# Kernel tuning notes

Hardware: AMD Instinct MI355X
Metric: run time of the kernel (lower is better)

Reference implementation:

```python
import jax, jax.numpy as jnp
import numpy as np

D = 1024      # model_dim
H = 2048      # expert hidden_dim
E = 8         # num routed experts
TOP_K = 2
N_SHARED = 1
B, S = 2, 1024


def setup_inputs() -> dict:
    key = jax.random.key(0)
    ks = jax.random.split(key, 12)
    sc = 0.02
    return {
        "hidden": jax.random.normal(ks[0], (B, S, D), jnp.float32),
        # router Linear(D -> E); stored as [in, out]
        "router_w": jax.random.normal(ks[1], (D, E), jnp.float32) * sc,
        "router_b": jnp.zeros((E,), jnp.float32),
        # shared expert (1): Linear(D->H), Linear(H->D)
        "sw1": jax.random.normal(ks[2], (D, H), jnp.float32) * sc,
        "sb1": jnp.zeros((H,), jnp.float32),
        "sw2": jax.random.normal(ks[3], (H, D), jnp.float32) * sc,
        "sb2": jnp.zeros((D,), jnp.float32),
        # routed experts, stacked over E
        "rw1": jax.random.normal(ks[4], (E, D, H), jnp.float32) * sc,
        "rb1": jnp.zeros((E, H), jnp.float32),
        "rw2": jax.random.normal(ks[5], (E, H, D), jnp.float32) * sc,
        "rb2": jnp.zeros((E, D), jnp.float32),
    }


def reference(hidden, router_w, router_b, sw1, sb1, sw2, sb2, rw1, rb1, rw2, rb2):
    b, s, d = hidden.shape
    T = b * s
    flat = hidden.reshape(T, d)                              # [T, D]

    # --- router ---
    router_logits = flat @ router_w + router_b               # [T, E]
    router_probs = jax.nn.softmax(router_logits, axis=-1)
    topk_probs, topk_idx = jax.lax.top_k(router_probs, TOP_K)  # [T, K]

    # per-(token, expert) mixing weight: sum of top-k probs that hit expert e
    weights = jnp.zeros_like(router_probs).at[
        jnp.arange(T)[:, None], topk_idx
    ].add(topk_probs)                                        # [T, E]

    # --- shared expert(s) (1 expert -> mean == itself) ---
    sh = jax.nn.gelu(flat @ sw1 + sb1, approximate=False)    # [T, H]
    shared_out = (sh @ sw2 + sb2) / N_SHARED                 # [T, D]

    # --- routed experts: dense all-expert eval weighted by routing weights ---
    # (identical math to the gather/FFN/index_add loop: weight is 0 for
    #  tokens not routed to expert e)
    h1 = jax.nn.gelu(jnp.einsum('td,edh->teh', flat, rw1) + rb1[None],
                     approximate=False)                      # [T, E, H]
    expert_out = jnp.einsum('teh,ehd->ted', h1, rw2) + rb2[None]  # [T, E, D]
    mixed = jnp.einsum('ted,te->td', expert_out, weights)    # [T, D]

    return (shared_out + mixed).reshape(b, s, d)
```

## Files before the change

### kernel.cpp

```cpp
#include <hip/hip_runtime.h>
#include <hip/hip_bf16.h>

#define T_TOK 2048
#define DDIM  1024
#define HDIM  2048
#define NEXP  8
#define NSEG  9

typedef unsigned short u16;
typedef __attribute__((ext_vector_type(4))) float f32x4;
typedef __attribute__((ext_vector_type(8))) short bf16x8;
typedef __attribute__((ext_vector_type(4))) unsigned short u16x4;

__device__ __forceinline__ u16 f2bf(float x) {
  union { float f; unsigned int u; } v; v.f = x;
  unsigned int r = v.u + 0x7fffu + ((v.u >> 16) & 1u);
  return (u16)(r >> 16);
}
__device__ __forceinline__ float gelu_exact(float x) {
  return 0.5f * x * (1.0f + erff(x * 0.70710678118654752f));
}
__device__ __forceinline__ int swz4(int row) {
  return (row & 3) ^ ((row >> 2) & 3);
}

__device__ __forceinline__ void gload16(const void* g, void* l) {
  __builtin_amdgcn_global_load_lds(
      (const __attribute__((address_space(1))) unsigned int*)g,
      (__attribute__((address_space(3))) unsigned int*)l, 16, 0, 0);
}

__global__ __launch_bounds__(256) void router_kernel(
    const float* __restrict__ x, const float* __restrict__ rw,
    const float* __restrict__ rb, u16* __restrict__ xb,
    float* __restrict__ weights, int* __restrict__ counts,
    int* __restrict__ lists)
{
  int wv = threadIdx.x >> 6, lane = threadIdx.x & 63;
  int t = blockIdx.x * 4 + wv;
  const float* xrow = x + (size_t)t * DDIM;
  float acc[NEXP];
#pragma unroll
  for (int e = 0; e < NEXP; e++) acc[e] = 0.f;
#pragma unroll
  for (int i = 0; i < 4; i++) {
    int d0 = i * 256 + lane * 4;
    f32x4 xv = *(const f32x4*)(xrow + d0);
    u16x4 pk;
#pragma unroll
    for (int j = 0; j < 4; j++) {
      float xs = xv[j];
      pk[j] = f2bf(xs);
      const float* wr = rw + (size_t)(d0 + j) * NEXP;
#pragma unroll
      for (int e = 0; e < NEXP; e++) acc[e] = fmaf(xs, wr[e], acc[e]);
    }
    *(u16x4*)(xb + (size_t)t * DDIM + d0) = pk;
  }
#pragma unroll
  for (int off = 32; off >= 1; off >>= 1)
#pragma unroll
    for (int e = 0; e < NEXP; e++) acc[e] += __shfl_xor(acc[e], off);

  if (lane == 0) {
    float lg[NEXP], mx = -1e30f;
#pragma unroll
    for (int e = 0; e < NEXP; e++) { lg[e] = acc[e] + rb[e]; mx = fmaxf(mx, lg[e]); }
    float p[NEXP], s = 0.f;
#pragma unroll
    for (int e = 0; e < NEXP; e++) { p[e] = expf(lg[e] - mx); s += p[e]; }
    float inv = 1.0f / s;
#pragma unroll
    for (int e = 0; e < NEXP; e++) p[e] *= inv;
    int i1 = 0;
#pragma unroll
    for (int e = 1; e < NEXP; e++) if (p[e] > p[i1]) i1 = e;
    int i2 = (i1 == 0) ? 1 : 0;
#pragma unroll
    for (int e = 0; e < NEXP; e++) if (e != i1 && p[e] > p[i2]) i2 = e;
#pragma unroll
    for (int e = 0; e < NEXP; e++)
      weights[(size_t)t * NEXP + e] = (e == i1) ? p[i1] : (e == i2) ? p[i2] : 0.f;
    int p1 = atomicAdd(counts + i1, 1); lists[i1 * T_TOK + p1] = t;
    int p2 = atomicAdd(counts + i2, 1); lists[i2 * T_TOK + p2] = t;
    lists[NEXP * T_TOK + t] = t;
  }
}

__global__ void seg_kernel(int* counts, int* segoff, int* ytab, int* nyt) {
  counts[NEXP] = T_TOK;
  int off = 0, n = 0;
  for (int e = 0; e < NSEG; e++) {
    segoff[e] = off;
    int c = counts[e];
    for (int my = 0; my * 256 < c; my++) ytab[n++] = e * 256 + my;
    off += c;
  }
  *nyt = n;
}

__global__ __launch_bounds__(256) void transpose_bf16_kernel(
    const float* __restrict__ rin, const float* __restrict__ sin_,
    u16* __restrict__ rout, u16* __restrict__ sout, int R, int C)
{
  __shared__ float tile[32][33];
  int b = blockIdx.z;
  const float* inb = (b < NEXP) ? rin + (size_t)b * R * C : sin_;
  u16* outb = (b < NEXP) ? rout + (size_t)b * R * C : sout;
  int r0 = blockIdx.y * 32, c0 = blockIdx.x * 32;
  int tx = threadIdx.x & 31, ty = threadIdx.x >> 5;
#pragma unroll
  for (int j = 0; j < 4; j++) {
    int r = ty + j * 8;
    tile[r][tx] = inb[(size_t)(r0 + r) * C + c0 + tx];
  }
  __syncthreads();
#pragma unroll
  for (int j = 0; j < 4; j++) {
    int rr = ty + j * 8;
    outb[(size_t)(c0 + rr) * R + r0 + tx] = f2bf(tile[tx][rr]);
  }
}


__global__ __launch_bounds__(512) void gemm1_kernel(
    const u16* __restrict__ Xb, const u16* __restrict__ rw1t,
    const u16* __restrict__ sw1t, const float* __restrict__ rb1,
    const float* __restrict__ sb1, const int* __restrict__ counts,
    const int* __restrict__ segoff, const int* __restrict__ lists,
    const int* __restrict__ ytab, const int* __restrict__ nyt,
    u16* __restrict__ H1)
{
  __shared__ u16 Alds[4][256 * 32];
  __shared__ u16 Blds[4][256 * 32];

  int tid = threadIdx.x, lane = tid & 63;
  int wv = tid >> 6, wm = wv >> 2, wn = wv & 3;
  int kc = lane >> 4, lr = lane & 15;

  int srow[2], soff[2];
#pragma unroll
  for (int j = 0; j < 2; j++) {
    int i = j * 512 + tid;
    srow[j] = i >> 2;
    soff[j] = (((i & 3) ^ swz4(i >> 2)) * 8);
  }
  int aoff[8], boff[4];
#pragma unroll
  for (int f = 0; f < 8; f++) {
    int ra = wm * 128 + f * 16 + lr;
    aoff[f] = ra * 32 + ((kc ^ swz4(ra)) * 8);
  }
#pragma unroll
  for (int f = 0; f < 4; f++) {
    int rb_ = wn * 64 + f * 16 + lr;
    boff[f] = rb_ * 32 + ((kc ^ swz4(rb_)) * 8);
  }

  int ntile = nyt[0] * (HDIM / 256);
  for (int t = blockIdx.x; t < ntile; t += gridDim.x) {
    int yt = t >> 3, nx = t & 7;
    int em = ytab[yt];
    int e = em >> 8, m0 = (em & 255) * 256, n0 = nx * 256;
    int cnt = counts[e];
    const u16* Bt = (e < NEXP) ? (rw1t + (size_t)e * HDIM * DDIM) : sw1t;
    const float* bias = (e < NEXP) ? (rb1 + (size_t)e * HDIM) : sb1;
    const int* list = lists + e * T_TOK;
    int seg = segoff[e];

    size_t abase[2], bbase[2];
#pragma unroll
    for (int j = 0; j < 2; j++) {
      int tok = list[min(m0 + srow[j], cnt - 1)];
      abase[j] = (size_t)tok * DDIM + soff[j];
      bbase[j] = (size_t)(n0 + srow[j]) * DDIM + soff[j];
    }

    f32x4 acc[8][4];
#pragma unroll
    for (int i = 0; i < 8; i++)
#pragma unroll
      for (int j = 0; j < 4; j++) acc[i][j] = (f32x4){0.f, 0.f, 0.f, 0.f};

    const int NS = DDIM / 32;
#pragma unroll
    for (int s = 0; s < 2; s++)
#pragma unroll
      for (int j = 0; j < 2; j++) {
        int i = j * 512 + tid;
        gload16(Xb + abase[j] + s * 32, &Alds[s][i * 8]);
        gload16(Bt + bbase[j] + s * 32, &Blds[s][i * 8]);
      }

    for (int s = 0; s < NS; s++) {
      if (s + 2 < NS) {
        int kk = (s + 2) * 32;
        int nb = (s + 2) & 3;
#pragma unroll
        for (int j = 0; j < 2; j++) {
          int i = j * 512 + tid;
          gload16(Xb + abase[j] + kk, &Alds[nb][i * 8]);
          gload16(Bt + bbase[j] + kk, &Blds[nb][i * 8]);
        }
        asm volatile("s_waitcnt vmcnt(8)" ::: "memory");
      } else if (s + 1 < NS) {
        asm volatile("s_waitcnt vmcnt(4)" ::: "memory");
      } else {
        asm volatile("s_waitcnt vmcnt(0)" ::: "memory");
      }
      __builtin_amdgcn_s_barrier();
      __builtin_amdgcn_sched_barrier(0);

      const u16* Ac = &Alds[s & 3][0];
      const u16* Bc = &Blds[s & 3][0];
      bf16x8 af[8], bfr[4];
#pragma unroll
      for (int f = 0; f < 8; f++) af[f] = *(const bf16x8*)(Ac + aoff[f]);
#pragma unroll
      for (int f = 0; f < 4; f++) bfr[f] = *(const bf16x8*)(Bc + boff[f]);
      __builtin_amdgcn_s_setprio(1);
#pragma unroll
      for (int mf = 0; mf < 8; mf++)
#pragma unroll
        for (int nf = 0; nf < 4; nf++)
          acc[mf][nf] = __builtin_amdgcn_mfma_f32_16x16x32_bf16(af[mf], bfr[nf], acc[mf][nf], 0, 0, 0);
      __builtin_amdgcn_s_setprio(0);
    }

#pragma unroll
    for (int nf = 0; nf < 4; nf++) {
      int col = n0 + wn * 64 + nf * 16 + lr;
      float b = bias[col];
#pragma unroll
      for (int mf = 0; mf < 8; mf++) {
#pragma unroll
        for (int rg = 0; rg < 4; rg++) {
          int mt = wm * 128 + mf * 16 + kc * 4 + rg;
          if (m0 + mt < cnt) {
            float v = acc[mf][nf][rg] + b;
            H1[(size_t)(seg + m0 + mt) * HDIM + col] = f2bf(gelu_exact(v));
          }
        }
      }
    }
    __builtin_amdgcn_s_barrier();
    __builtin_amdgcn_sched_barrier(0);
  }
}

__global__ __launch_bounds__(512) void gemm2_kernel(
    const u16* __restrict__ H1, const u16* __restrict__ rw2t,
    const u16* __restrict__ sw2t, const float* __restrict__ rb2,
    const float* __restrict__ sb2, const float* __restrict__ weights,
    const int* __restrict__ counts, const int* __restrict__ segoff,
    const int* __restrict__ lists, const int* __restrict__ ytab,
    const int* __restrict__ nyt, float* __restrict__ out)
{
  __shared__ u16 Alds[4][256 * 32];
  __shared__ u16 Blds[4][256 * 32];

  int tid = threadIdx.x, lane = tid & 63;
  int wv = tid >> 6, wm = wv >> 2, wn = wv & 3;
  int kc = lane >> 4, lr = lane & 15;

  int srow[2], soff[2];
#pragma unroll
  for (int j = 0; j < 2; j++) {
    int i = j * 512 + tid;
    srow[j] = i >> 2;
    soff[j] = (((i & 3) ^ swz4(i >> 2)) * 8);
  }
  int aoff[8], boff[4];
#pragma unroll
  for (int f = 0; f < 8; f++) {
    int ra = wm * 128 + f * 16 + lr;
    aoff[f] = ra * 32 + ((kc ^ swz4(ra)) * 8);
  }
#pragma unroll
  for (int f = 0; f < 4; f++) {
    int rb_ = wn * 64 + f * 16 + lr;
    boff[f] = rb_ * 32 + ((kc ^ swz4(rb_)) * 8);
  }

  int ntile = nyt[0] * (DDIM / 256) * 2;
  for (int t = blockIdx.x; t < ntile; t += gridDim.x) {
    int kh = t & 1, nx = (t >> 1) & 3, yt = t >> 3;
    int em = ytab[yt];
    int e = em >> 8, m0 = (em & 255) * 256, n0 = nx * 256;
    int cnt = counts[e];
    const u16* Bt = (e < NEXP) ? (rw2t + (size_t)e * DDIM * HDIM) : sw2t;
    const float* bias = (e < NEXP) ? (rb2 + (size_t)e * DDIM) : sb2;
    const int* list = lists + e * T_TOK;
    int seg = segoff[e];
    int k0 = kh * 1024;

    size_t abase[2], bbase[2];
#pragma unroll
    for (int j = 0; j < 2; j++) {
      abase[j] = (size_t)(seg + min(m0 + srow[j], cnt - 1)) * HDIM + k0 + soff[j];
      bbase[j] = (size_t)(n0 + srow[j]) * HDIM + k0 + soff[j];
    }

    f32x4 acc[8][4];
#pragma unroll
    for (int i = 0; i < 8; i++)
#pragma unroll
      for (int j = 0; j < 4; j++) acc[i][j] = (f32x4){0.f, 0.f, 0.f, 0.f};

    const int NS = 1024 / 32;
#pragma unroll
    for (int s = 0; s < 2; s++)
#pragma unroll
      for (int j = 0; j < 2; j++) {
        int i = j * 512 + tid;
        gload16(H1 + abase[j] + s * 32, &Alds[s][i * 8]);
        gload16(Bt + bbase[j] + s * 32, &Blds[s][i * 8]);
      }

    for (int s = 0; s < NS; s++) {
      if (s + 2 < NS) {
        int kk = (s + 2) * 32;
        int nb = (s + 2) & 3;
#pragma unroll
        for (int j = 0; j < 2; j++) {
          int i = j * 512 + tid;
          gload16(H1 + abase[j] + kk, &Alds[nb][i * 8]);
          gload16(Bt + bbase[j] + kk, &Blds[nb][i * 8]);
        }
        asm volatile("s_waitcnt vmcnt(8)" ::: "memory");
      } else if (s + 1 < NS) {
        asm volatile("s_waitcnt vmcnt(4)" ::: "memory");
      } else {
        asm volatile("s_waitcnt vmcnt(0)" ::: "memory");
      }
      __builtin_amdgcn_s_barrier();
      __builtin_amdgcn_sched_barrier(0);

      const u16* Ac = &Alds[s & 3][0];
      const u16* Bc = &Blds[s & 3][0];
      bf16x8 af[8], bfr[4];
#pragma unroll
      for (int f = 0; f < 8; f++) af[f] = *(const bf16x8*)(Ac + aoff[f]);
#pragma unroll
      for (int f = 0; f < 4; f++) bfr[f] = *(const bf16x8*)(Bc + boff[f]);
      __builtin_amdgcn_s_setprio(1);
#pragma unroll
      for (int mf = 0; mf < 8; mf++)
#pragma unroll
        for (int nf = 0; nf < 4; nf++)
          acc[mf][nf] = __builtin_amdgcn_mfma_f32_16x16x32_bf16(af[mf], bfr[nf], acc[mf][nf], 0, 0, 0);
      __builtin_amdgcn_s_setprio(0);
    }

    float biasv[4];
#pragma unroll
    for (int nf = 0; nf < 4; nf++)
      biasv[nf] = (kh == 0) ? bias[n0 + wn * 64 + nf * 16 + lr] : 0.f;

#pragma unroll
    for (int mf = 0; mf < 8; mf++) {
#pragma unroll
      for (int rg = 0; rg < 4; rg++) {
        int mt = wm * 128 + mf * 16 + kc * 4 + rg;
        int mrow = m0 + mt;
        if (mrow < cnt) {
          int tok = list[mrow];
          float w = (e < NEXP) ? weights[(size_t)tok * NEXP + e] : 1.0f;
          float* orow = out + (size_t)tok * DDIM + n0 + wn * 64 + lr;
#pragma unroll
          for (int nf = 0; nf < 4; nf++)
            atomicAdd(orow + nf * 16, w * (acc[mf][nf][rg] + biasv[nf]));
        }
      }
    }
    __builtin_amdgcn_s_barrier();
    __builtin_amdgcn_sched_barrier(0);
  }
}

extern "C" void kernel_launch(void* const* d_in, const int* in_sizes, int n_in,
                              void* d_out, int out_size, void* d_ws, size_t ws_size,
                              hipStream_t stream) {
  (void)in_sizes; (void)n_in; (void)out_size; (void)ws_size;
  const float* hidden   = (const float*)d_in[0];
  const float* router_w = (const float*)d_in[1];
  const float* router_b = (const float*)d_in[2];
  const float* sw1 = (const float*)d_in[3];
  const float* sb1 = (const float*)d_in[4];
  const float* sw2 = (const float*)d_in[5];
  const float* sb2 = (const float*)d_in[6];
  const float* rw1 = (const float*)d_in[7];
  const float* rb1 = (const float*)d_in[8];
  const float* rw2 = (const float*)d_in[9];
  const float* rb2 = (const float*)d_in[10];
  float* out = (float*)d_out;

  char* ws = (char*)d_ws;
  u16* Xb      = (u16*)(ws + 0);
  u16* rw1t    = (u16*)(ws + 4194304);
  u16* rw2t    = (u16*)(ws + 37748736);
  u16* sw1t    = (u16*)(ws + 71303168);
  u16* sw2t    = (u16*)(ws + 75497472);
  u16* H1      = (u16*)(ws + 79691776);
  float* weights = (float*)(ws + 104857600);
  int* counts  = (int*)(ws + 104923136);
  int* segoff  = (int*)(ws + 104923200);
  int* lists   = (int*)(ws + 104923264);
  int* ytab    = (int*)(ws + 104996992);
  int* nyt     = (int*)(ws + 104997632);

  hipMemsetAsync(counts, 0, 64, stream);
  hipMemsetAsync(out, 0, (size_t)T_TOK * DDIM * sizeof(float), stream);

  router_kernel<<<T_TOK / 4, 256, 0, stream>>>(hidden, router_w, router_b, Xb,
                                               weights, counts, lists);
  seg_kernel<<<1, 1, 0, stream>>>(counts, segoff, ytab, nyt);

  transpose_bf16_kernel<<<dim3(HDIM / 32, DDIM / 32, NSEG), 256, 0, stream>>>(
      rw1, sw1, rw1t, sw1t, DDIM, HDIM);
  transpose_bf16_kernel<<<dim3(DDIM / 32, HDIM / 32, NSEG), 256, 0, stream>>>(
      rw2, sw2, rw2t, sw2t, HDIM, DDIM);

  gemm1_kernel<<<256, 512, 0, stream>>>(
      Xb, rw1t, sw1t, rb1, sb1, counts, segoff, lists, ytab, nyt, H1);
  gemm2_kernel<<<256, 512, 0, stream>>>(
      H1, rw2t, sw2t, rb2, sb2, weights, counts, segoff, lists, ytab, nyt, out);
}
```

Baseline: 248.9 us.

## Pre-gather routed tokens contiguously and assign GEMM tiles per XCD

```diff
diff --git a/kernel.cpp b/kernel.cpp
--- a/kernel.cpp
+++ b/kernel.cpp
@@ -99,6 +99,22 @@
   *nyt = n;
 }
 
+__global__ __launch_bounds__(256) void gather_kernel(
+    const u16* __restrict__ xb, const int* __restrict__ lists,
+    const int* __restrict__ counts, const int* __restrict__ segoff,
+    u16* __restrict__ xg)
+{
+  int e = blockIdx.y;
+  int cnt = counts[e], seg = segoff[e];
+  const int* list = lists + e * T_TOK;
+  int tid = threadIdx.x;
+  for (int r = blockIdx.x; r < cnt; r += gridDim.x) {
+    int tok = list[r];
+    *(u16x4*)(xg + (size_t)(seg + r) * DDIM + tid * 4) =
+        *(const u16x4*)(xb + (size_t)tok * DDIM + tid * 4);
+  }
+}
+
 __global__ __launch_bounds__(256) void transpose_bf16_kernel(
     const float* __restrict__ rin, const float* __restrict__ sin_,
     u16* __restrict__ rout, u16* __restrict__ sout, int R, int C)
@@ -122,14 +138,23 @@
   }
 }
 
+__device__ __forceinline__ void xcd_range(int ntile, int& start, int& cntx,
+                                          int& pos, int& stride) {
+  int q = ntile >> 3, r = ntile & 7;
+  int xcd = blockIdx.x & 7;
+  pos = blockIdx.x >> 3;
+  stride = gridDim.x >> 3;
+  start = (xcd < r) ? xcd * (q + 1) : r * (q + 1) + (xcd - r) * q;
+  cntx = q + ((xcd < r) ? 1 : 0);
+}
+
 
 __global__ __launch_bounds__(512) void gemm1_kernel(
-    const u16* __restrict__ Xb, const u16* __restrict__ rw1t,
+    const u16* __restrict__ Xg, const u16* __restrict__ rw1t,
     const u16* __restrict__ sw1t, const float* __restrict__ rb1,
     const float* __restrict__ sb1, const int* __restrict__ counts,
-    const int* __restrict__ segoff, const int* __restrict__ lists,
-    const int* __restrict__ ytab, const int* __restrict__ nyt,
-    u16* __restrict__ H1)
+    const int* __restrict__ segoff, const int* __restrict__ ytab,
+    const int* __restrict__ nyt, u16* __restrict__ H1)
 {
   __shared__ u16 Alds[4][256 * 32];
   __shared__ u16 Blds[4][256 * 32];
@@ -158,21 +183,22 @@
   }
 
   int ntile = nyt[0] * (HDIM / 256);
-  for (int t = blockIdx.x; t < ntile; t += gridDim.x) {
+  int start, cntx, pos, stride;
+  xcd_range(ntile, start, cntx, pos, stride);
+  for (int p = pos; p < cntx; p += stride) {
+    int t = start + p;
     int yt = t >> 3, nx = t & 7;
     int em = ytab[yt];
     int e = em >> 8, m0 = (em & 255) * 256, n0 = nx * 256;
     int cnt = counts[e];
     const u16* Bt = (e < NEXP) ? (rw1t + (size_t)e * HDIM * DDIM) : sw1t;
     const float* bias = (e < NEXP) ? (rb1 + (size_t)e * HDIM) : sb1;
-    const int* list = lists + e * T_TOK;
     int seg = segoff[e];
 
     size_t abase[2], bbase[2];
 #pragma unroll
     for (int j = 0; j < 2; j++) {
-      int tok = list[min(m0 + srow[j], cnt - 1)];
-      abase[j] = (size_t)tok * DDIM + soff[j];
+      abase[j] = (size_t)(seg + min(m0 + srow[j], cnt - 1)) * DDIM + soff[j];
       bbase[j] = (size_t)(n0 + srow[j]) * DDIM + soff[j];
     }
 
@@ -188,7 +214,7 @@
 #pragma unroll
       for (int j = 0; j < 2; j++) {
         int i = j * 512 + tid;
-        gload16(Xb + abase[j] + s * 32, &Alds[s][i * 8]);
+        gload16(Xg + abase[j] + s * 32, &Alds[s][i * 8]);
         gload16(Bt + bbase[j] + s * 32, &Blds[s][i * 8]);
       }
 
@@ -199,7 +225,7 @@
 #pragma unroll
         for (int j = 0; j < 2; j++) {
           int i = j * 512 + tid;
-          gload16(Xb + abase[j] + kk, &Alds[nb][i * 8]);
+          gload16(Xg + abase[j] + kk, &Alds[nb][i * 8]);
           gload16(Bt + bbase[j] + kk, &Blds[nb][i * 8]);
         }
         asm volatile("s_waitcnt vmcnt(8)" ::: "memory");
@@ -283,7 +309,10 @@
   }
 
   int ntile = nyt[0] * (DDIM / 256) * 2;
-  for (int t = blockIdx.x; t < ntile; t += gridDim.x) {
+  int start, cntx, pos, stride;
+  xcd_range(ntile, start, cntx, pos, stride);
+  for (int p = pos; p < cntx; p += stride) {
+    int t = start + p;
     int kh = t & 1, nx = (t >> 1) & 3, yt = t >> 3;
     int em = ytab[yt];
     int e = em >> 8, m0 = (em & 255) * 256, n0 = nx * 256;
@@ -399,6 +428,7 @@
   u16* Xb      = (u16*)(ws + 0);
   u16* rw1t    = (u16*)(ws + 4194304);
   u16* rw2t    = (u16*)(ws + 37748736);
+  u16* Xg      = (u16*)(ws + 37748736);
   u16* sw1t    = (u16*)(ws + 71303168);
   u16* sw2t    = (u16*)(ws + 75497472);
   u16* H1      = (u16*)(ws + 79691776);
@@ -418,11 +448,15 @@
 
   transpose_bf16_kernel<<<dim3(HDIM / 32, DDIM / 32, NSEG), 256, 0, stream>>>(
       rw1, sw1, rw1t, sw1t, DDIM, HDIM);
+
+  gather_kernel<<<dim3(64, NSEG), 256, 0, stream>>>(Xb, lists, counts, segoff, Xg);
+
+  gemm1_kernel<<<256, 512, 0, stream>>>(
+      Xg, rw1t, sw1t, rb1, sb1, counts, segoff, ytab, nyt, H1);
+
   transpose_bf16_kernel<<<dim3(DDIM / 32, HDIM / 32, NSEG), 256, 0, stream>>>(
       rw2, sw2, rw2t, sw2t, HDIM, DDIM);
 
-  gemm1_kernel<<<256, 512, 0, stream>>>(
-      Xb, rw1t, sw1t, rb1, sb1, counts, segoff, lists, ytab, nyt, H1);
   gemm2_kernel<<<256, 512, 0, stream>>>(
       H1, rw2t, sw2t, rb2, sb2, weights, counts, segoff, lists, ytab, nyt, out);
 }
```

Result: slower. 277.1 us (+11.3%).

## Fuse fp32 weight transpose and bf16 conversion into expert GEMM loaders

Applied to the files above, without the earlier changes.

```diff
diff --git a/kernel.cpp b/kernel.cpp
--- a/kernel.cpp
+++ b/kernel.cpp
@@ -99,40 +99,17 @@
   *nyt = n;
 }
 
-__global__ __launch_bounds__(256) void transpose_bf16_kernel(
-    const float* __restrict__ rin, const float* __restrict__ sin_,
-    u16* __restrict__ rout, u16* __restrict__ sout, int R, int C)
-{
-  __shared__ float tile[32][33];
-  int b = blockIdx.z;
-  const float* inb = (b < NEXP) ? rin + (size_t)b * R * C : sin_;
-  u16* outb = (b < NEXP) ? rout + (size_t)b * R * C : sout;
-  int r0 = blockIdx.y * 32, c0 = blockIdx.x * 32;
-  int tx = threadIdx.x & 31, ty = threadIdx.x >> 5;
-#pragma unroll
-  for (int j = 0; j < 4; j++) {
-    int r = ty + j * 8;
-    tile[r][tx] = inb[(size_t)(r0 + r) * C + c0 + tx];
-  }
-  __syncthreads();
-#pragma unroll
-  for (int j = 0; j < 4; j++) {
-    int rr = ty + j * 8;
-    outb[(size_t)(c0 + rr) * R + r0 + tx] = f2bf(tile[tx][rr]);
-  }
-}
-
 
 __global__ __launch_bounds__(512) void gemm1_kernel(
-    const u16* __restrict__ Xb, const u16* __restrict__ rw1t,
-    const u16* __restrict__ sw1t, const float* __restrict__ rb1,
+    const u16* __restrict__ Xb, const float* __restrict__ rw1,
+    const float* __restrict__ sw1, const float* __restrict__ rb1,
     const float* __restrict__ sb1, const int* __restrict__ counts,
     const int* __restrict__ segoff, const int* __restrict__ lists,
     const int* __restrict__ ytab, const int* __restrict__ nyt,
     u16* __restrict__ H1)
 {
   __shared__ u16 Alds[4][256 * 32];
-  __shared__ u16 Blds[4][256 * 32];
+  __shared__ u16 Blds[2][256 * 32];
 
   int tid = threadIdx.x, lane = tid & 63;
   int wv = tid >> 6, wm = wv >> 2, wn = wv & 3;
@@ -156,6 +133,10 @@
     int rb_ = wn * 64 + f * 16 + lr;
     boff[f] = rb_ * 32 + ((kc ^ swz4(rb_)) * 8);
   }
+  int bw[4];
+#pragma unroll
+  for (int j = 0; j < 4; j++)
+    bw[j] = ((lane << 2) + j) * 32 + (((wv >> 1) ^ j ^ (lane & 3)) << 3) + ((wv & 1) << 2);
 
   int ntile = nyt[0] * (HDIM / 256);
   for (int t = blockIdx.x; t < ntile; t += gridDim.x) {
@@ -163,18 +144,18 @@
     int em = ytab[yt];
     int e = em >> 8, m0 = (em & 255) * 256, n0 = nx * 256;
     int cnt = counts[e];
-    const u16* Bt = (e < NEXP) ? (rw1t + (size_t)e * HDIM * DDIM) : sw1t;
+    const float* Wf = (e < NEXP) ? (rw1 + (size_t)e * DDIM * HDIM) : sw1;
     const float* bias = (e < NEXP) ? (rb1 + (size_t)e * HDIM) : sb1;
     const int* list = lists + e * T_TOK;
     int seg = segoff[e];
 
-    size_t abase[2], bbase[2];
+    size_t abase[2];
 #pragma unroll
     for (int j = 0; j < 2; j++) {
       int tok = list[min(m0 + srow[j], cnt - 1)];
       abase[j] = (size_t)tok * DDIM + soff[j];
-      bbase[j] = (size_t)(n0 + srow[j]) * DDIM + soff[j];
-    }
+    }
+    const float* Wb = Wf + n0 + (lane << 2);
 
     f32x4 acc[8][4];
 #pragma unroll
@@ -183,13 +164,20 @@
       for (int j = 0; j < 4; j++) acc[i][j] = (f32x4){0.f, 0.f, 0.f, 0.f};
 
     const int NS = DDIM / 32;
+    f32x4 vBa, vBb, vBc, vBd;
+    {
+      const float* Wk = Wb + (size_t)(wv * 4) * HDIM;
+      vBa = *(const f32x4*)(Wk);
+      vBb = *(const f32x4*)(Wk + HDIM);
+      vBc = *(const f32x4*)(Wk + 2 * HDIM);
+      vBd = *(const f32x4*)(Wk + 3 * HDIM);
+    }
 #pragma unroll
     for (int s = 0; s < 2; s++)
 #pragma unroll
       for (int j = 0; j < 2; j++) {
         int i = j * 512 + tid;
         gload16(Xb + abase[j] + s * 32, &Alds[s][i * 8]);
-        gload16(Bt + bbase[j] + s * 32, &Blds[s][i * 8]);
       }
 
     for (int s = 0; s < NS; s++) {
@@ -200,19 +188,34 @@
         for (int j = 0; j < 2; j++) {
           int i = j * 512 + tid;
           gload16(Xb + abase[j] + kk, &Alds[nb][i * 8]);
-          gload16(Bt + bbase[j] + kk, &Blds[nb][i * 8]);
-        }
-        asm volatile("s_waitcnt vmcnt(8)" ::: "memory");
-      } else if (s + 1 < NS) {
-        asm volatile("s_waitcnt vmcnt(4)" ::: "memory");
-      } else {
-        asm volatile("s_waitcnt vmcnt(0)" ::: "memory");
-      }
+        }
+      }
+      {
+        u16* Bd = &Blds[s & 1][0];
+#pragma unroll
+        for (int j = 0; j < 4; j++) {
+          u16x4 pk;
+          pk[0] = f2bf(vBa[j]); pk[1] = f2bf(vBb[j]);
+          pk[2] = f2bf(vBc[j]); pk[3] = f2bf(vBd[j]);
+          *(u16x4*)(Bd + bw[j]) = pk;
+        }
+      }
+      if (s + 1 < NS) {
+        const float* Wk = Wb + (size_t)((s + 1) * 32 + wv * 4) * HDIM;
+        vBa = *(const f32x4*)(Wk);
+        vBb = *(const f32x4*)(Wk + HDIM);
+        vBc = *(const f32x4*)(Wk + 2 * HDIM);
+        vBd = *(const f32x4*)(Wk + 3 * HDIM);
+      }
+      if (s + 2 < NS)      asm volatile("s_waitcnt vmcnt(8)" ::: "memory");
+      else if (s + 1 < NS) asm volatile("s_waitcnt vmcnt(6)" ::: "memory");
+      else                 asm volatile("s_waitcnt vmcnt(0)" ::: "memory");
+      asm volatile("s_waitcnt lgkmcnt(0)" ::: "memory");
       __builtin_amdgcn_s_barrier();
       __builtin_amdgcn_sched_barrier(0);
 
       const u16* Ac = &Alds[s & 3][0];
-      const u16* Bc = &Blds[s & 3][0];
+      const u16* Bc = &Blds[s & 1][0];
       bf16x8 af[8], bfr[4];
 #pragma unroll
       for (int f = 0; f < 8; f++) af[f] = *(const bf16x8*)(Ac + aoff[f]);
@@ -249,15 +252,15 @@
 }
 
 __global__ __launch_bounds__(512) void gemm2_kernel(
-    const u16* __restrict__ H1, const u16* __restrict__ rw2t,
-    const u16* __restrict__ sw2t, const float* __restrict__ rb2,
+    const u16* __restrict__ H1, const float* __restrict__ rw2,
+    const float* __restrict__ sw2, const float* __restrict__ rb2,
     const float* __restrict__ sb2, const float* __restrict__ weights,
     const int* __restrict__ counts, const int* __restrict__ segoff,
     const int* __restrict__ lists, const int* __restrict__ ytab,
     const int* __restrict__ nyt, float* __restrict__ out)
 {
   __shared__ u16 Alds[4][256 * 32];
-  __shared__ u16 Blds[4][256 * 32];
+  __shared__ u16 Blds[2][256 * 32];
 
   int tid = threadIdx.x, lane = tid & 63;
   int wv = tid >> 6, wm = wv >> 2, wn = wv & 3;
@@ -281,6 +284,10 @@
     int rb_ = wn * 64 + f * 16 + lr;
     boff[f] = rb_ * 32 + ((kc ^ swz4(rb_)) * 8);
   }
+  int bw[4];
+#pragma unroll
+  for (int j = 0; j < 4; j++)
+    bw[j] = ((lane << 2) + j) * 32 + (((wv >> 1) ^ j ^ (lane & 3)) << 3) + ((wv & 1) << 2);
 
   int ntile = nyt[0] * (DDIM / 256) * 2;
   for (int t = blockIdx.x; t < ntile; t += gridDim.x) {
@@ -288,18 +295,17 @@
     int em = ytab[yt];
     int e = em >> 8, m0 = (em & 255) * 256, n0 = nx * 256;
     int cnt = counts[e];
-    const u16* Bt = (e < NEXP) ? (rw2t + (size_t)e * DDIM * HDIM) : sw2t;
+    const float* Wf = (e < NEXP) ? (rw2 + (size_t)e * HDIM * DDIM) : sw2;
     const float* bias = (e < NEXP) ? (rb2 + (size_t)e * DDIM) : sb2;
     const int* list = lists + e * T_TOK;
     int seg = segoff[e];
     int k0 = kh * 1024;
 
-    size_t abase[2], bbase[2];
-#pragma unroll
-    for (int j = 0; j < 2; j++) {
+    size_t abase[2];
+#pragma unroll
+    for (int j = 0; j < 2; j++)
       abase[j] = (size_t)(seg + min(m0 + srow[j], cnt - 1)) * HDIM + k0 + soff[j];
-      bbase[j] = (size_t)(n0 + srow[j]) * HDIM + k0 + soff[j];
-    }
+    const float* Wb = Wf + (size_t)k0 * DDIM + n0 + (lane << 2);
 
     f32x4 acc[8][4];
 #pragma unroll
@@ -308,13 +314,20 @@
       for (int j = 0; j < 4; j++) acc[i][j] = (f32x4){0.f, 0.f, 0.f, 0.f};
 
     const int NS = 1024 / 32;
+    f32x4 vBa, vBb, vBc, vBd;
+    {
+      const float* Wk = Wb + (size_t)(wv * 4) * DDIM;
+      vBa = *(const f32x4*)(Wk);
+      vBb = *(const f32x4*)(Wk + DDIM);
+      vBc = *(const f32x4*)(Wk + 2 * DDIM);
+      vBd = *(const f32x4*)(Wk + 3 * DDIM);
+    }
 #pragma unroll
     for (int s = 0; s < 2; s++)
 #pragma unroll
       for (int j = 0; j < 2; j++) {
         int i = j * 512 + tid;
         gload16(H1 + abase[j] + s * 32, &Alds[s][i * 8]);
-        gload16(Bt + bbase[j] + s * 32, &Blds[s][i * 8]);
       }
 
     for (int s = 0; s < NS; s++) {
@@ -325,19 +338,34 @@
         for (int j = 0; j < 2; j++) {
           int i = j * 512 + tid;
           gload16(H1 + abase[j] + kk, &Alds[nb][i * 8]);
-          gload16(Bt + bbase[j] + kk, &Blds[nb][i * 8]);
-        }
-        asm volatile("s_waitcnt vmcnt(8)" ::: "memory");
-      } else if (s + 1 < NS) {
-        asm volatile("s_waitcnt vmcnt(4)" ::: "memory");
-      } else {
-        asm volatile("s_waitcnt vmcnt(0)" ::: "memory");
-      }
+        }
+      }
+      {
+        u16* Bd = &Blds[s & 1][0];
+#pragma unroll
+        for (int j = 0; j < 4; j++) {
+          u16x4 pk;
+          pk[0] = f2bf(vBa[j]); pk[1] = f2bf(vBb[j]);
+          pk[2] = f2bf(vBc[j]); pk[3] = f2bf(vBd[j]);
+          *(u16x4*)(Bd + bw[j]) = pk;
+        }
+      }
+      if (s + 1 < NS) {
+        const float* Wk = Wb + (size_t)((s + 1) * 32 + wv * 4) * DDIM;
+        vBa = *(const f32x4*)(Wk);
+        vBb = *(const f32x4*)(Wk + DDIM);
+        vBc = *(const f32x4*)(Wk + 2 * DDIM);
+        vBd = *(const f32x4*)(Wk + 3 * DDIM);
+      }
+      if (s + 2 < NS)      asm volatile("s_waitcnt vmcnt(8)" ::: "memory");
+      else if (s + 1 < NS) asm volatile("s_waitcnt vmcnt(6)" ::: "memory");
+      else                 asm volatile("s_waitcnt vmcnt(0)" ::: "memory");
+      asm volatile("s_waitcnt lgkmcnt(0)" ::: "memory");
       __builtin_amdgcn_s_barrier();
       __builtin_amdgcn_sched_barrier(0);
 
       const u16* Ac = &Alds[s & 3][0];
-      const u16* Bc = &Blds[s & 3][0];
+      const u16* Bc = &Blds[s & 1][0];
       bf16x8 af[8], bfr[4];
 #pragma unroll
       for (int f = 0; f < 8; f++) af[f] = *(const bf16x8*)(Ac + aoff[f]);
@@ -397,17 +425,13 @@
 
   char* ws = (char*)d_ws;
   u16* Xb      = (u16*)(ws + 0);
-  u16* rw1t    = (u16*)(ws + 4194304);
-  u16* rw2t    = (u16*)(ws + 37748736);
-  u16* sw1t    = (u16*)(ws + 71303168);
-  u16* sw2t    = (u16*)(ws + 75497472);
-  u16* H1      = (u16*)(ws + 79691776);
-  float* weights = (float*)(ws + 104857600);
-  int* counts  = (int*)(ws + 104923136);
-  int* segoff  = (int*)(ws + 104923200);
-  int* lists   = (int*)(ws + 104923264);
-  int* ytab    = (int*)(ws + 104996992);
-  int* nyt     = (int*)(ws + 104997632);
+  u16* H1      = (u16*)(ws + 4194304);
+  float* weights = (float*)(ws + 29360128);
+  int* counts  = (int*)(ws + 29425664);
+  int* segoff  = (int*)(ws + 29425728);
+  int* lists   = (int*)(ws + 29425792);
+  int* ytab    = (int*)(ws + 29499520);
+  int* nyt     = (int*)(ws + 29500160);
 
   hipMemsetAsync(counts, 0, 64, stream);
   hipMemsetAsync(out, 0, (size_t)T_TOK * DDIM * sizeof(float), stream);
@@ -416,13 +440,8 @@
                                                weights, counts, lists);
   seg_kernel<<<1, 1, 0, stream>>>(counts, segoff, ytab, nyt);
 
-  transpose_bf16_kernel<<<dim3(HDIM / 32, DDIM / 32, NSEG), 256, 0, stream>>>(
-      rw1, sw1, rw1t, sw1t, DDIM, HDIM);
-  transpose_bf16_kernel<<<dim3(DDIM / 32, HDIM / 32, NSEG), 256, 0, stream>>>(
-      rw2, sw2, rw2t, sw2t, HDIM, DDIM);
-
   gemm1_kernel<<<256, 512, 0, stream>>>(
-      Xb, rw1t, sw1t, rb1, sb1, counts, segoff, lists, ytab, nyt, H1);
+      Xb, rw1, sw1, rb1, sb1, counts, segoff, lists, ytab, nyt, H1);
   gemm2_kernel<<<256, 512, 0, stream>>>(
-      H1, rw2t, sw2t, rb2, sb2, weights, counts, segoff, lists, ytab, nyt, out);
-}
+      H1, rw2, sw2, rb2, sb2, weights, counts, segoff, lists, ytab, nyt, out);
+}
```

After: 229.3 us. 1.09x faster.
